# Optimization experiments

Measured on AMD Instinct MI355X. Metric: run time of the kernel, lower is better.

The kernel has to match this reference:

```python
import jax, jax.numpy as jnp
import numpy as np
from jax import lax

B, T, H, E, V, ENC = 2048, 48, 512, 256, 128, 1024


def setup_inputs() -> dict:
    key = jax.random.key(0)
    ks = jax.random.split(key, 13)
    s = 0.05  # weight scale to keep activations sane
    return {
        "tgt_ids": jax.random.randint(ks[0], (B, T), 0, V),
        "enc_hid": jax.random.normal(ks[1], (B, ENC), jnp.float32),
        "W_init1": s * jax.random.normal(ks[2], (ENC, H), jnp.float32),
        "W_init2": s * jax.random.normal(ks[3], (ENC, H), jnp.float32),
        "embed_table": s * jax.random.normal(ks[4], (V, E), jnp.float32),
        "k1": s * jax.random.normal(ks[5], (E, 3 * H), jnp.float32),
        "rk1": s * jax.random.normal(ks[6], (H, 3 * H), jnp.float32),
        "b1": jnp.zeros((2, 3 * H), jnp.float32),
        "k2": s * jax.random.normal(ks[7], (H, 3 * H), jnp.float32),
        "rk2": s * jax.random.normal(ks[8], (H, 3 * H), jnp.float32),
        "b2": jnp.zeros((2, 3 * H), jnp.float32),
        "Wv": s * jax.random.normal(ks[9], (H, V), jnp.float32),
        "bv": jnp.zeros((V,), jnp.float32),
    }


def gru_masked(x_proj, mask, h0, rk, rb):
    """Keras GRU (reset_after=True, gate order z,r,h) with mask carry-through.
    x_proj: [B,T,3H] precomputed x@kernel + input_bias. mask: [B,T] bool.
    Masked steps keep previous state AND previous output (Keras masking semantics;
    GRU output == state)."""
    def step(h, inp):
        xg, m = inp  # xg: [B,3H], m: [B]
        inner = h @ rk + rb  # [B,3H]
        xz, xr, xh = jnp.split(xg, 3, axis=-1)
        rz, rr, rh = jnp.split(inner, 3, axis=-1)
        z = jax.nn.sigmoid(xz + rz)
        r = jax.nn.sigmoid(xr + rr)
        hh = jnp.tanh(xh + r * rh)
        h_new = z * h + (1.0 - z) * hh
        h = jnp.where(m[:, None], h_new, h)
        return h, h

    _, seq = lax.scan(step, h0, (x_proj.transpose(1, 0, 2), mask.T))
    return seq.transpose(1, 0, 2)  # [B,T,H]


def reference(tgt_ids, enc_hid, W_init1, W_init2, embed_table,
              k1, rk1, b1, k2, rk2, b2, Wv, bv):
    mask = tgt_ids != 0  # mask_zero=True
    emb = embed_table[tgt_ids]  # [B,T,E]
    h01 = enc_hid @ W_init1  # Dense no-bias init of layer-1 state
    h02 = enc_hid @ W_init2
    x1 = emb @ k1 + b1[0]  # [B,T,3H]
    seq1 = gru_masked(x1, mask, h01, rk1, b1[1])
    x2 = seq1 @ k2 + b2[0]
    seq2 = gru_masked(x2, mask, h02, rk2, b2[1])
    probs = jax.nn.softmax(seq2 @ Wv + bv, axis=-1)  # [B,T,V]
    return probs
```

## Files before the change

kernel.cpp:

```cpp
#include <hip/hip_runtime.h>
#include <hip/hip_bf16.h>
#include <math.h>

#define B_   2048
#define T_   48
#define H_   512
#define E_   256
#define V_   128
#define ENC_ 1024
#define H3_  1536
#define BH_  (B_ * H_)

typedef __attribute__((ext_vector_type(8))) short bf16x8;
typedef __attribute__((ext_vector_type(4))) float f32x4;
typedef unsigned short ushort_t;

#if defined(__has_builtin)
#if __has_builtin(__builtin_amdgcn_global_load_lds)
#define HAVE_ASYNC 1
#endif
#endif
#ifndef HAVE_ASYNC
#define HAVE_ASYNC 0
#endif

__device__ __forceinline__ void stage16(const ushort_t* g, ushort_t* l, int lane)
{
#if HAVE_ASYNC
    __builtin_amdgcn_global_load_lds(
        (const __attribute__((address_space(1))) unsigned int*)g,
        (__attribute__((address_space(3))) unsigned int*)l, 16, 0, 0);
#else
    *(bf16x8*)(l + lane * 8) = *(const bf16x8*)g;
#endif
}

__device__ __forceinline__ float sigmoidf_(float x) { return 1.0f / (1.0f + expf(-x)); }

constexpr int BM = 64, BN = 64, BK = 16;

__device__ __forceinline__ void gemm_f32_body(
    const float* __restrict__ A, const float* __restrict__ Bm,
    const float* __restrict__ bias, float* __restrict__ C,
    int M, int N, int K)
{
    __shared__ float As[BK][BM + 4];
    __shared__ float Bs[BK][BN + 4];

    const int tid = threadIdx.x;
    const int bm = blockIdx.y * BM;
    const int bn = blockIdx.x * BN;
    const int tm = (tid >> 4) * 4;
    const int tn = (tid & 15) * 4;
    const int lmA = tid >> 2;
    const int lkA = (tid & 3) * 4;
    const int lkB = tid >> 4;
    const int lnB = (tid & 15) * 4;

    float acc[4][4] = {};

    for (int k0 = 0; k0 < K; k0 += BK) {
        float4 av  = *(const float4*)(A  + (size_t)(bm + lmA) * K + (k0 + lkA));
        float4 bv4 = *(const float4*)(Bm + (size_t)(k0 + lkB) * N + (bn + lnB));
        As[lkA + 0][lmA] = av.x;
        As[lkA + 1][lmA] = av.y;
        As[lkA + 2][lmA] = av.z;
        As[lkA + 3][lmA] = av.w;
        *(float4*)&Bs[lkB][lnB] = bv4;
        __syncthreads();

        #pragma unroll
        for (int k = 0; k < BK; ++k) {
            float4 a = *(const float4*)&As[k][tm];
            float4 b = *(const float4*)&Bs[k][tn];
            acc[0][0] += a.x * b.x; acc[0][1] += a.x * b.y; acc[0][2] += a.x * b.z; acc[0][3] += a.x * b.w;
            acc[1][0] += a.y * b.x; acc[1][1] += a.y * b.y; acc[1][2] += a.y * b.z; acc[1][3] += a.y * b.w;
            acc[2][0] += a.z * b.x; acc[2][1] += a.z * b.y; acc[2][2] += a.z * b.z; acc[2][3] += a.z * b.w;
            acc[3][0] += a.w * b.x; acc[3][1] += a.w * b.y; acc[3][2] += a.w * b.z; acc[3][3] += a.w * b.w;
        }
        __syncthreads();
    }

    #pragma unroll
    for (int r = 0; r < 4; ++r)
        #pragma unroll
        for (int c = 0; c < 4; ++c) {
            float v = acc[r][c];
            if (bias) v += bias[bn + tn + c];
            C[(size_t)(bm + tm + r) * N + (bn + tn + c)] = v;
        }
}

__global__ __launch_bounds__(256) void gemm_f32(
    const float* __restrict__ A, const float* __restrict__ Bm,
    const float* __restrict__ bias, float* __restrict__ C,
    int M, int N, int K)
{
    gemm_f32_body(A, Bm, bias, C, M, N, K);
}

__global__ __launch_bounds__(256) void gemm_init2(
    const float* __restrict__ A, const float* __restrict__ B0,
    const float* __restrict__ B1, float* __restrict__ C0, float* __restrict__ C1,
    int M, int N, int K)
{
    const float* Bm = blockIdx.z ? B1 : B0;
    float*       C  = blockIdx.z ? C1 : C0;
    gemm_f32_body(A, Bm, nullptr, C, M, N, K);
}

__global__ __launch_bounds__(256) void transpose_to_bf16(
    const float* __restrict__ W, __hip_bfloat16* __restrict__ Wt, int K, int N)
{
    __shared__ float tile[32][33];
    const int bk = blockIdx.y * 32, bn = blockIdx.x * 32;
    const int tx = threadIdx.x & 31, ty = threadIdx.x >> 5;
    #pragma unroll
    for (int i = ty; i < 32; i += 8)
        tile[i][tx] = W[(size_t)(bk + i) * N + (bn + tx)];
    __syncthreads();
    #pragma unroll
    for (int i = ty; i < 32; i += 8)
        Wt[(size_t)(bn + i) * K + (bk + tx)] = __float2bfloat16(tile[tx][i]);
}

__global__ __launch_bounds__(256) void f32_to_bf16_k(
    const float* __restrict__ a, __hip_bfloat16* __restrict__ o, int n)
{
    int idx = blockIdx.x * 256 + threadIdx.x;
    if (idx < n) o[idx] = __float2bfloat16(a[idx]);
}

__global__ __launch_bounds__(256, 2) void l1_fused(
    const int* __restrict__ tgt, int t,
    const float* __restrict__ xe1,
    const ushort_t* __restrict__ rkt,
    const float* __restrict__ rb,
    const float* __restrict__ hf_cur, const ushort_t* __restrict__ hb_cur,
    float* __restrict__ hf_nxt, __hip_bfloat16* __restrict__ hb_nxt)
{
    __shared__ __attribute__((aligned(16))) ushort_t Al[2][4096];
    __shared__ __attribute__((aligned(16))) ushort_t Bl[2][6144];

    const int tid  = threadIdx.x;
    const int lane = tid & 63;
    const int w    = tid >> 6;
    const int ln   = lane & 15;
    const int kg   = lane >> 4;
    const int wr   = w >> 1, wc = w & 1;

    const int lin = blockIdx.y * 16 + blockIdx.x;
    const int swz = (lin & 7) * 64 + (lin >> 3);
    const int m0  = (swz >> 4) * 64;
    const int i0  = (swz & 15) * 32;

    const int crow = lane >> 3;
    const int ckof = ((lane & 7) ^ crow) * 8;
    const int i    = i0 + wc * 16 + ln;

    const float rbz = rb[i], rbr = rb[H_ + i], rbh = rb[2 * H_ + i];
    int   ids[2][4];
    float hvs[2][4];
    #pragma unroll
    for (int fm = 0; fm < 2; ++fm)
        #pragma unroll
        for (int r = 0; r < 4; ++r) {
            const int b = m0 + wr * 32 + fm * 16 + kg * 4 + r;
            ids[fm][r] = tgt[(size_t)b * T_ + t];
            hvs[fm][r] = hf_cur[(size_t)b * H_ + i];
        }
    float xgz[2][4], xgr[2][4], xgh[2][4];
    #pragma unroll
    for (int fm = 0; fm < 2; ++fm)
        #pragma unroll
        for (int r = 0; r < 4; ++r) {
            const float* xg = xe1 + (size_t)ids[fm][r] * H3_;
            xgz[fm][r] = xg[i]; xgr[fm][r] = xg[H_ + i]; xgh[fm][r] = xg[2 * H_ + i];
        }

    const int ko0 = (kg * 8) ^ ((ln & 7) * 8);
    const int ko1 = (32 + kg * 8) ^ ((ln & 7) * 8);

    f32x4 acc[2][3] = {};

    auto STAGE = [&](int pb, int k0) {
        #pragma unroll
        for (int c = w; c < 20; c += 4) {
            const ushort_t* g; ushort_t* l;
            if (c < 8) {
                g = hb_cur + (size_t)(m0 + c * 8 + crow) * H_ + k0 + ckof;
                l = &Al[pb][c * 512];
            } else {
                const int idx = c - 8;
                g = rkt + (size_t)((idx >> 2) * H_ + i0 + (idx & 3) * 8 + crow) * H_ + k0 + ckof;
                l = &Bl[pb][idx * 512];
            }
            stage16(g, l, lane);
        }
    };

    STAGE(0, 0);
    __syncthreads();
    int buf = 0;
    for (int k0 = 0; k0 < H_; k0 += 64) {
        if (k0 + 64 < H_) STAGE(buf ^ 1, k0 + 64);
        #pragma unroll
        for (int kk = 0; kk < 2; ++kk) {
            const int ko = kk ? ko1 : ko0;
            bf16x8 af[2], bf[3];
            #pragma unroll
            for (int fm = 0; fm < 2; ++fm)
                af[fm] = *(const bf16x8*)(&Al[buf][(wr * 32 + fm * 16 + ln) * 64 + ko]);
            #pragma unroll
            for (int g = 0; g < 3; ++g)
                bf[g] = *(const bf16x8*)(&Bl[buf][g * 2048 + (wc * 16 + ln) * 64 + ko]);
            #pragma unroll
            for (int fm = 0; fm < 2; ++fm)
                #pragma unroll
                for (int g = 0; g < 3; ++g)
                    acc[fm][g] = __builtin_amdgcn_mfma_f32_16x16x32_bf16(
                        af[fm], bf[g], acc[fm][g], 0, 0, 0);
        }
        __syncthreads();
        buf ^= 1;
    }

    #pragma unroll
    for (int fm = 0; fm < 2; ++fm)
        #pragma unroll
        for (int r = 0; r < 4; ++r) {
            const int b = m0 + wr * 32 + fm * 16 + kg * 4 + r;
            const float hv = hvs[fm][r];
            float z  = sigmoidf_(xgz[fm][r] + acc[fm][0][r] + rbz);
            float rr = sigmoidf_(xgr[fm][r] + acc[fm][1][r] + rbr);
            float hh = tanhf(xgh[fm][r] + rr * (acc[fm][2][r] + rbh));
            float hn = (ids[fm][r] != 0) ? (z * hv + (1.0f - z) * hh) : hv;
            hf_nxt[(size_t)b * H_ + i] = hn;
            hb_nxt[(size_t)b * H_ + i] = __float2bfloat16(hn);
        }
}

__global__ __launch_bounds__(256, 2) void l2_fused(
    const int* __restrict__ tgt, int t,
    const ushort_t* __restrict__ k2t,
    const ushort_t* __restrict__ rk2t,
    const float* __restrict__ bx,
    const float* __restrict__ br,
    const ushort_t* __restrict__ s1b,
    const float* __restrict__ hf_cur,
    const ushort_t* __restrict__ hb_cur, size_t hbs,
    float* __restrict__ hf_nxt,
    __hip_bfloat16* __restrict__ hbo, size_t hos)
{
    __shared__ __attribute__((aligned(16))) ushort_t A0l[2][4096];
    __shared__ __attribute__((aligned(16))) ushort_t A1l[2][4096];
    __shared__ __attribute__((aligned(16))) ushort_t B0l[6144];
    __shared__ __attribute__((aligned(16))) ushort_t B1l[6144];

    const int tid  = threadIdx.x;
    const int lane = tid & 63;
    const int w    = tid >> 6;
    const int ln   = lane & 15;
    const int kg   = lane >> 4;
    const int wr   = w >> 1, wc = w & 1;

    const int lin = blockIdx.y * 16 + blockIdx.x;
    const int swz = (lin & 7) * 64 + (lin >> 3);
    const int m0  = (swz >> 4) * 64;
    const int i0  = (swz & 15) * 32;

    const int crow = lane >> 3;
    const int ckof = ((lane & 7) ^ crow) * 8;
    const int i    = i0 + wc * 16 + ln;

    const float bxz = bx[i], bxr = bx[H_ + i], bxh = bx[2 * H_ + i];
    const float brz = br[i], brr = br[H_ + i], brh = br[2 * H_ + i];
    int   ids[2][4];
    float hvs[2][4];
    #pragma unroll
    for (int fm = 0; fm < 2; ++fm)
        #pragma unroll
        for (int r = 0; r < 4; ++r) {
            const int b = m0 + wr * 32 + fm * 16 + kg * 4 + r;
            ids[fm][r] = tgt[(size_t)b * T_ + t];
            hvs[fm][r] = hf_cur[(size_t)b * H_ + i];
        }

    const int ko0 = (kg * 8) ^ ((ln & 7) * 8);
    const int ko1 = (32 + kg * 8) ^ ((ln & 7) * 8);

    auto STAGE_A = [&](int pb, int k0) {
        #pragma unroll
        for (int c = w; c < 16; c += 4) {
            const ushort_t* g; ushort_t* l;
            if (c < 8) {
                g = s1b + (size_t)(m0 + c * 8 + crow) * H_ + k0 + ckof;
                l = &A0l[pb][c * 512];
            } else {
                const int cc = c - 8;
                g = hb_cur + (size_t)(m0 + cc * 8 + crow) * hbs + k0 + ckof;
                l = &A1l[pb][cc * 512];
            }
            stage16(g, l, lane);
        }
    };
    auto STAGE_B = [&](int k0) {
        #pragma unroll
        for (int c = w; c < 24; c += 4) {
            const ushort_t* g; ushort_t* l;
            if (c < 12) {
                g = k2t + (size_t)((c >> 2) * H_ + i0 + (c & 3) * 8 + crow) * H_ + k0 + ckof;
                l = &B0l[c * 512];
            } else {
                const int idx = c - 12;
                g = rk2t + (size_t)((idx >> 2) * H_ + i0 + (idx & 3) * 8 + crow) * H_ + k0 + ckof;
                l = &B1l[idx * 512];
            }
            stage16(g, l, lane);
        }
    };

    f32x4 acc0[2][3] = {};
    f32x4 acc1[2][3] = {};

    STAGE_A(0, 0);
    STAGE_B(0);
    __syncthreads();
    int buf = 0;
    for (int k0 = 0; k0 < H_; k0 += 64) {
        const bool more = (k0 + 64 < H_);
        if (more) STAGE_A(buf ^ 1, k0 + 64);

        bf16x8 a0f[2][2], a1f[2][2], b0f[2][3], b1f[2][3];
        #pragma unroll
        for (int kk = 0; kk < 2; ++kk) {
            const int ko = kk ? ko1 : ko0;
            #pragma unroll
            for (int fm = 0; fm < 2; ++fm) {
                a0f[kk][fm] = *(const bf16x8*)(&A0l[buf][(wr * 32 + fm * 16 + ln) * 64 + ko]);
                a1f[kk][fm] = *(const bf16x8*)(&A1l[buf][(wr * 32 + fm * 16 + ln) * 64 + ko]);
            }
            #pragma unroll
            for (int g = 0; g < 3; ++g) {
                b0f[kk][g] = *(const bf16x8*)(&B0l[g * 2048 + (wc * 16 + ln) * 64 + ko]);
                b1f[kk][g] = *(const bf16x8*)(&B1l[g * 2048 + (wc * 16 + ln) * 64 + ko]);
            }
        }
        __builtin_amdgcn_sched_barrier(0);
        asm volatile("s_waitcnt lgkmcnt(0)" ::: "memory");
        __builtin_amdgcn_sched_barrier(0);
        __builtin_amdgcn_s_barrier();
        if (more) STAGE_B(k0 + 64);

        #pragma unroll
        for (int kk = 0; kk < 2; ++kk)
            #pragma unroll
            for (int fm = 0; fm < 2; ++fm)
                #pragma unroll
                for (int g = 0; g < 3; ++g) {
                    acc0[fm][g] = __builtin_amdgcn_mfma_f32_16x16x32_bf16(
                        a0f[kk][fm], b0f[kk][g], acc0[fm][g], 0, 0, 0);
                    acc1[fm][g] = __builtin_amdgcn_mfma_f32_16x16x32_bf16(
                        a1f[kk][fm], b1f[kk][g], acc1[fm][g], 0, 0, 0);
                }
        __syncthreads();
        buf ^= 1;
    }

    #pragma unroll
    for (int fm = 0; fm < 2; ++fm)
        #pragma unroll
        for (int r = 0; r < 4; ++r) {
            const int b = m0 + wr * 32 + fm * 16 + kg * 4 + r;
            const float hv = hvs[fm][r];
            float z  = sigmoidf_((acc0[fm][0][r] + bxz) + (acc1[fm][0][r] + brz));
            float rr = sigmoidf_((acc0[fm][1][r] + bxr) + (acc1[fm][1][r] + brr));
            float hh = tanhf((acc0[fm][2][r] + bxh) + rr * (acc1[fm][2][r] + brh));
            float hn = (ids[fm][r] != 0) ? (z * hv + (1.0f - z) * hh) : hv;
            hf_nxt[(size_t)b * H_ + i] = hn;
            hbo[(size_t)b * hos + i] = __float2bfloat16(hn);
        }
}

__device__ __forceinline__ void softmax_write4(
    float ax, float ay, float az, float aw, float* __restrict__ outp, int cg)
{
    float m = fmaxf(fmaxf(ax, ay), fmaxf(az, aw));
    #pragma unroll
    for (int d = 16; d >= 1; d >>= 1) m = fmaxf(m, __shfl_xor(m, d));
    float ex = __expf(ax - m), ey = __expf(ay - m),
          ez = __expf(az - m), ew = __expf(aw - m);
    float s = ex + ey + ez + ew;
    #pragma unroll
    for (int d = 16; d >= 1; d >>= 1) s += __shfl_xor(s, d);
    float inv = 1.0f / s;
    float4 o; o.x = ex * inv; o.y = ey * inv; o.z = ez * inv; o.w = ew * inv;
    *(float4*)(outp + cg * 4) = o;
}

__global__ __launch_bounds__(256) void out_softmax(
    const float* __restrict__ h2, const float* __restrict__ Wv,
    const float* __restrict__ bv, float* __restrict__ out, int t)
{
    const int tid = threadIdx.x;
    const int cg = tid & 31;
    const int rg = tid >> 5;
    const int row0 = blockIdx.x * 16;

    __shared__ float hs[16][512];
    for (int idx = tid; idx < 16 * 512; idx += 256)
        hs[idx >> 9][idx & 511] = h2[(size_t)(row0 + (idx >> 9)) * 512 + (idx & 511)];
    __syncthreads();

    const int r0 = rg * 2;
    const float4 bvv = *(const float4*)(bv + cg * 4);
    float a0x = bvv.x, a0y = bvv.y, a0z = bvv.z, a0w = bvv.w;
    float a1x = bvv.x, a1y = bvv.y, a1z = bvv.z, a1w = bvv.w;

    #pragma unroll 4
    for (int k = 0; k < 512; ++k) {
        float4 wv = *(const float4*)(Wv + (size_t)k * V_ + cg * 4);
        float h0 = hs[r0][k], h1 = hs[r0 + 1][k];
        a0x += h0 * wv.x; a0y += h0 * wv.y; a0z += h0 * wv.z; a0w += h0 * wv.w;
        a1x += h1 * wv.x; a1y += h1 * wv.y; a1z += h1 * wv.z; a1w += h1 * wv.w;
    }

    softmax_write4(a0x, a0y, a0z, a0w, out + ((size_t)(row0 + r0) * T_ + t) * V_, cg);
    softmax_write4(a1x, a1y, a1z, a1w, out + ((size_t)(row0 + r0 + 1) * T_ + t) * V_, cg);
}

__global__ __launch_bounds__(256) void proj_mfma(
    const ushort_t* __restrict__ s2, const ushort_t* __restrict__ wvt,
    const float* __restrict__ bv, float* __restrict__ out)
{
    const int lane = threadIdx.x & 63;
    const int w    = threadIdx.x >> 6;
    const int ln   = lane & 15;
    const int kg   = lane >> 4;
    const size_t row0 = (size_t)blockIdx.x * 128 + (size_t)w * 32;

    float bvl[8];
    #pragma unroll
    for (int nf = 0; nf < 8; ++nf) bvl[nf] = bv[nf * 16 + ln];

    f32x4 acc[2][8] = {};
    #pragma unroll 2
    for (int k0 = 0; k0 < H_; k0 += 32) {
        bf16x8 af[2], bf[8];
        #pragma unroll
        for (int mf = 0; mf < 2; ++mf)
            af[mf] = *(const bf16x8*)(s2 + (row0 + mf * 16 + ln) * H_ + k0 + kg * 8);
        #pragma unroll
        for (int nf = 0; nf < 8; ++nf)
            bf[nf] = *(const bf16x8*)(wvt + (size_t)(nf * 16 + ln) * H_ + k0 + kg * 8);
        #pragma unroll
        for (int mf = 0; mf < 2; ++mf)
            #pragma unroll
            for (int nf = 0; nf < 8; ++nf)
                acc[mf][nf] = __builtin_amdgcn_mfma_f32_16x16x32_bf16(
                    af[mf], bf[nf], acc[mf][nf], 0, 0, 0);
    }

    #pragma unroll
    for (int mf = 0; mf < 2; ++mf)
        #pragma unroll
        for (int q = 0; q < 4; ++q) {
            float v[8];
            float m = -1e30f;
            #pragma unroll
            for (int nf = 0; nf < 8; ++nf) { v[nf] = acc[mf][nf][q] + bvl[nf]; m = fmaxf(m, v[nf]); }
            #pragma unroll
            for (int d = 1; d <= 8; d <<= 1) m = fmaxf(m, __shfl_xor(m, d));
            float s = 0.f;
            #pragma unroll
            for (int nf = 0; nf < 8; ++nf) { v[nf] = __expf(v[nf] - m); s += v[nf]; }
            #pragma unroll
            for (int d = 1; d <= 8; d <<= 1) s += __shfl_xor(s, d);
            const float inv = 1.0f / s;
            float* op = out + (row0 + mf * 16 + kg * 4 + q) * V_;
            #pragma unroll
            for (int nf = 0; nf < 8; ++nf) op[nf * 16 + ln] = v[nf] * inv;
        }
}

extern "C" void kernel_launch(void* const* d_in, const int* in_sizes, int n_in,
                              void* d_out, int out_size, void* d_ws, size_t ws_size,
                              hipStream_t stream)
{
    const int*   tgt  = (const int*)  d_in[0];
    const float* enc  = (const float*)d_in[1];
    const float* Wi1  = (const float*)d_in[2];
    const float* Wi2  = (const float*)d_in[3];
    const float* emb  = (const float*)d_in[4];
    const float* k1   = (const float*)d_in[5];
    const float* rk1  = (const float*)d_in[6];
    const float* b1   = (const float*)d_in[7];
    const float* k2   = (const float*)d_in[8];
    const float* rk2  = (const float*)d_in[9];
    const float* b2   = (const float*)d_in[10];
    const float* Wv   = (const float*)d_in[11];
    const float* bv   = (const float*)d_in[12];
    float* out = (float*)d_out;

    float* ws  = (float*)d_ws;
    float* xe1 = ws;
    float* h1f = xe1 + (size_t)V_ * H3_;
    float* h2f = h1f + (size_t)2 * BH_;
    __hip_bfloat16* h1b = (__hip_bfloat16*)(h2f + (size_t)2 * BH_);
    __hip_bfloat16* h2b = h1b + (size_t)2 * BH_;
    __hip_bfloat16* rk1t = h2b + (size_t)2 * BH_;
    __hip_bfloat16* k2t  = rk1t + (size_t)H3_ * H_;
    __hip_bfloat16* rk2t = k2t  + (size_t)H3_ * H_;
    __hip_bfloat16* wvt  = rk2t + (size_t)H3_ * H_;
    __hip_bfloat16* seq2b = wvt + (size_t)V_ * H_;

    const size_t need = (size_t)((char*)(seq2b + (size_t)B_ * T_ * H_) - (char*)d_ws);
    const bool batched = ws_size >= need;

    dim3 blk(256);

    transpose_to_bf16<<<dim3(H3_ / 32, H_ / 32), blk, 0, stream>>>(rk1, rk1t, H_, H3_);
    transpose_to_bf16<<<dim3(H3_ / 32, H_ / 32), blk, 0, stream>>>(k2,  k2t,  H_, H3_);
    transpose_to_bf16<<<dim3(H3_ / 32, H_ / 32), blk, 0, stream>>>(rk2, rk2t, H_, H3_);
    if (batched)
        transpose_to_bf16<<<dim3(V_ / 32, H_ / 32), blk, 0, stream>>>(Wv, wvt, H_, V_);

    gemm_f32<<<dim3(H3_ / BN, V_ / BM), blk, 0, stream>>>(emb, k1, b1, xe1, V_, H3_, E_);
    gemm_init2<<<dim3(H_ / BN, B_ / BM, 2), blk, 0, stream>>>(enc, Wi1, Wi2, h1f, h2f, B_, H_, ENC_);
    f32_to_bf16_k<<<BH_ / 256, blk, 0, stream>>>(h1f, h1b, BH_);
    f32_to_bf16_k<<<BH_ / 256, blk, 0, stream>>>(h2f, h2b, BH_);

    const dim3 fgrid(H_ / 32, B_ / 64);

    for (int t = 0; t < T_; ++t) {
        const int cur = t & 1, nxt = cur ^ 1;
        float* h1f_c = h1f + (size_t)cur * BH_;
        float* h1f_n = h1f + (size_t)nxt * BH_;
        float* h2f_c = h2f + (size_t)cur * BH_;
        float* h2f_n = h2f + (size_t)nxt * BH_;
        __hip_bfloat16* h1b_c = h1b + (size_t)cur * BH_;
        __hip_bfloat16* h1b_n = h1b + (size_t)nxt * BH_;

        l1_fused<<<fgrid, blk, 0, stream>>>(
            tgt, t, xe1, (const ushort_t*)rk1t, b1 + H3_,
            h1f_c, (const ushort_t*)h1b_c, h1f_n, h1b_n);

        const ushort_t* hb_c; size_t hbs;
        __hip_bfloat16* hbo; size_t hos;
        if (batched) {
            hb_c = (t == 0) ? (const ushort_t*)h2b
                            : (const ushort_t*)(seq2b + (size_t)(t - 1) * H_);
            hbs  = (t == 0) ? (size_t)H_ : (size_t)T_ * H_;
            hbo  = seq2b + (size_t)t * H_;
            hos  = (size_t)T_ * H_;
        } else {
            hb_c = (const ushort_t*)(h2b + (size_t)cur * BH_); hbs = H_;
            hbo  = h2b + (size_t)nxt * BH_;                    hos = H_;
        }

        l2_fused<<<fgrid, blk, 0, stream>>>(
            tgt, t, (const ushort_t*)k2t, (const ushort_t*)rk2t, b2, b2 + H3_,
            (const ushort_t*)h1b_n, h2f_c, hb_c, hbs, h2f_n, hbo, hos);

        if (!batched)
            out_softmax<<<dim3(B_ / 16), blk, 0, stream>>>(h2f_n, Wv, bv, out, t);
    }

    if (batched)
        proj_mfma<<<dim3((B_ * T_) / 128), blk, 0, stream>>>(
            (const ushort_t*)seq2b, (const ushort_t*)wvt, bv, out);
}
```

Baseline: 1.540 ms.

## Fuse GRU time loop into persistent kernel with grid barriers; MFMA init GEMM

Replaces the 96 per-timestep kernel launches (l1_fused/l2_fused per step) with a single persistent kernel of 512 blocks that loops over timesteps and synchronises with an atomic-based grid barrier between layer phases. It also replaces the fp32 SIMT init-state GEMM plus separate bf16 casts with a split-bf16 (hi/lo, three MFMAs) MFMA GEMM that writes both fp32 and bf16 states directly. The aim is to remove launch overhead and the slow fp32 init GEMM. The persistent path relies on all 512 blocks being co-resident, which is checked once via an occupancy query, and adds grid-barrier spin costs.

```diff
diff --git a/kernel.cpp b/kernel.cpp
--- a/kernel.cpp
+++ b/kernel.cpp
@@ -10,6 +10,7 @@
 #define ENC_ 1024
 #define H3_  1536
 #define BH_  (B_ * H_)
+#define NBLK_ 512
 
 typedef __attribute__((ext_vector_type(8))) short bf16x8;
 typedef __attribute__((ext_vector_type(4))) float f32x4;
@@ -39,7 +40,7 @@
 
 constexpr int BM = 64, BN = 64, BK = 16;
 
-__device__ __forceinline__ void gemm_f32_body(
+__global__ __launch_bounds__(256) void gemm_f32(
     const float* __restrict__ A, const float* __restrict__ Bm,
     const float* __restrict__ bias, float* __restrict__ C,
     int M, int N, int K)
@@ -91,24 +92,6 @@
         }
 }
 
-__global__ __launch_bounds__(256) void gemm_f32(
-    const float* __restrict__ A, const float* __restrict__ Bm,
-    const float* __restrict__ bias, float* __restrict__ C,
-    int M, int N, int K)
-{
-    gemm_f32_body(A, Bm, bias, C, M, N, K);
-}
-
-__global__ __launch_bounds__(256) void gemm_init2(
-    const float* __restrict__ A, const float* __restrict__ B0,
-    const float* __restrict__ B1, float* __restrict__ C0, float* __restrict__ C1,
-    int M, int N, int K)
-{
-    const float* Bm = blockIdx.z ? B1 : B0;
-    float*       C  = blockIdx.z ? C1 : C0;
-    gemm_f32_body(A, Bm, nullptr, C, M, N, K);
-}
-
 __global__ __launch_bounds__(256) void transpose_to_bf16(
     const float* __restrict__ W, __hip_bfloat16* __restrict__ Wt, int K, int N)
 {
@@ -124,23 +107,58 @@
         Wt[(size_t)(bn + i) * K + (bk + tx)] = __float2bfloat16(tile[tx][i]);
 }
 
-__global__ __launch_bounds__(256) void f32_to_bf16_k(
-    const float* __restrict__ a, __hip_bfloat16* __restrict__ o, int n)
-{
-    int idx = blockIdx.x * 256 + threadIdx.x;
-    if (idx < n) o[idx] = __float2bfloat16(a[idx]);
-}
-
-__global__ __launch_bounds__(256, 2) void l1_fused(
-    const int* __restrict__ tgt, int t,
-    const float* __restrict__ xe1,
-    const ushort_t* __restrict__ rkt,
-    const float* __restrict__ rb,
-    const float* __restrict__ hf_cur, const ushort_t* __restrict__ hb_cur,
-    float* __restrict__ hf_nxt, __hip_bfloat16* __restrict__ hb_nxt)
-{
-    __shared__ __attribute__((aligned(16))) ushort_t Al[2][4096];
-    __shared__ __attribute__((aligned(16))) ushort_t Bl[2][6144];
+__global__ __launch_bounds__(256) void transpose_split(
+    const float* __restrict__ W, __hip_bfloat16* __restrict__ Whi,
+    __hip_bfloat16* __restrict__ Wlo, int K, int N)
+{
+    __shared__ float tile[32][33];
+    const int bk = blockIdx.y * 32, bn = blockIdx.x * 32;
+    const int tx = threadIdx.x & 31, ty = threadIdx.x >> 5;
+    #pragma unroll
+    for (int i = ty; i < 32; i += 8)
+        tile[i][tx] = W[(size_t)(bk + i) * N + (bn + tx)];
+    __syncthreads();
+    #pragma unroll
+    for (int i = ty; i < 32; i += 8) {
+        const float v = tile[tx][i];
+        const __hip_bfloat16 h = __float2bfloat16(v);
+        Whi[(size_t)(bn + i) * K + (bk + tx)] = h;
+        Wlo[(size_t)(bn + i) * K + (bk + tx)] = __float2bfloat16(v - __bfloat162float(h));
+    }
+}
+
+__global__ __launch_bounds__(256) void split_cast(
+    const float* __restrict__ x, __hip_bfloat16* __restrict__ hi,
+    __hip_bfloat16* __restrict__ lo, int n)
+{
+    const int i0 = (blockIdx.x * 256 + threadIdx.x) * 4;
+    if (i0 >= n) return;
+    const float4 v = *(const float4*)(x + i0);
+    const float vv[4] = { v.x, v.y, v.z, v.w };
+    #pragma unroll
+    for (int j = 0; j < 4; ++j) {
+        const __hip_bfloat16 h = __float2bfloat16(vv[j]);
+        hi[i0 + j] = h;
+        lo[i0 + j] = __float2bfloat16(vv[j] - __bfloat162float(h));
+    }
+}
+
+__global__ __launch_bounds__(256, 2) void init_mfma(
+    const ushort_t* __restrict__ ehi, const ushort_t* __restrict__ elo,
+    const ushort_t* __restrict__ w1hi, const ushort_t* __restrict__ w1lo,
+    const ushort_t* __restrict__ w2hi, const ushort_t* __restrict__ w2lo,
+    float* __restrict__ h1f, __hip_bfloat16* __restrict__ h1b,
+    float* __restrict__ h2f, __hip_bfloat16* __restrict__ h2b)
+{
+    const ushort_t* whi = blockIdx.z ? w2hi : w1hi;
+    const ushort_t* wlo = blockIdx.z ? w2lo : w1lo;
+    float* hf = blockIdx.z ? h2f : h1f;
+    __hip_bfloat16* hb = blockIdx.z ? h2b : h1b;
+
+    __shared__ __attribute__((aligned(16))) ushort_t Ahi[2][4096];
+    __shared__ __attribute__((aligned(16))) ushort_t Alo[2][4096];
+    __shared__ __attribute__((aligned(16))) ushort_t Bhi[2][2048];
+    __shared__ __attribute__((aligned(16))) ushort_t Blo[2][2048];
 
     const int tid  = threadIdx.x;
     const int lane = tid & 63;
@@ -148,8 +166,93 @@
     const int ln   = lane & 15;
     const int kg   = lane >> 4;
     const int wr   = w >> 1, wc = w & 1;
-
-    const int lin = blockIdx.y * 16 + blockIdx.x;
+    const int m0   = blockIdx.y * 64;
+    const int i0   = blockIdx.x * 32;
+
+    const int crow = lane >> 3;
+    const int ckof = ((lane & 7) ^ crow) * 8;
+    const int ko0 = (kg * 8) ^ ((ln & 7) * 8);
+    const int ko1 = (32 + kg * 8) ^ ((ln & 7) * 8);
+
+    auto STG = [&](int pb, int k0) {
+        #pragma unroll
+        for (int c = w; c < 24; c += 4) {
+            const ushort_t* g; ushort_t* l;
+            if (c < 8) {
+                g = ehi + (size_t)(m0 + c * 8 + crow) * ENC_ + k0 + ckof;
+                l = &Ahi[pb][c * 512];
+            } else if (c < 16) {
+                const int cc = c - 8;
+                g = elo + (size_t)(m0 + cc * 8 + crow) * ENC_ + k0 + ckof;
+                l = &Alo[pb][cc * 512];
+            } else if (c < 20) {
+                const int cc = c - 16;
+                g = whi + (size_t)(i0 + cc * 8 + crow) * ENC_ + k0 + ckof;
+                l = &Bhi[pb][cc * 512];
+            } else {
+                const int cc = c - 20;
+                g = wlo + (size_t)(i0 + cc * 8 + crow) * ENC_ + k0 + ckof;
+                l = &Blo[pb][cc * 512];
+            }
+            stage16(g, l, lane);
+        }
+    };
+
+    f32x4 acc[2] = {};
+    STG(0, 0);
+    __syncthreads();
+    int buf = 0;
+    for (int k0 = 0; k0 < ENC_; k0 += 64) {
+        if (k0 + 64 < ENC_) STG(buf ^ 1, k0 + 64);
+        #pragma unroll
+        for (int kk = 0; kk < 2; ++kk) {
+            const int ko = kk ? ko1 : ko0;
+            bf16x8 ah[2], al[2], bh, bl;
+            #pragma unroll
+            for (int fm = 0; fm < 2; ++fm) {
+                ah[fm] = *(const bf16x8*)(&Ahi[buf][(wr * 32 + fm * 16 + ln) * 64 + ko]);
+                al[fm] = *(const bf16x8*)(&Alo[buf][(wr * 32 + fm * 16 + ln) * 64 + ko]);
+            }
+            bh = *(const bf16x8*)(&Bhi[buf][(wc * 16 + ln) * 64 + ko]);
+            bl = *(const bf16x8*)(&Blo[buf][(wc * 16 + ln) * 64 + ko]);
+            #pragma unroll
+            for (int fm = 0; fm < 2; ++fm) {
+                acc[fm] = __builtin_amdgcn_mfma_f32_16x16x32_bf16(ah[fm], bh, acc[fm], 0, 0, 0);
+                acc[fm] = __builtin_amdgcn_mfma_f32_16x16x32_bf16(al[fm], bh, acc[fm], 0, 0, 0);
+                acc[fm] = __builtin_amdgcn_mfma_f32_16x16x32_bf16(ah[fm], bl, acc[fm], 0, 0, 0);
+            }
+        }
+        __syncthreads();
+        buf ^= 1;
+    }
+
+    const int i = i0 + wc * 16 + ln;
+    #pragma unroll
+    for (int fm = 0; fm < 2; ++fm)
+        #pragma unroll
+        for (int r = 0; r < 4; ++r) {
+            const int b = m0 + wr * 32 + fm * 16 + kg * 4 + r;
+            const float v = acc[fm][r];
+            hf[(size_t)b * H_ + i] = v;
+            hb[(size_t)b * H_ + i] = __float2bfloat16(v);
+        }
+}
+
+__device__ __forceinline__ void l1_phase(
+    ushort_t* Al0, ushort_t* Bl0,
+    int lin, int t,
+    const int* __restrict__ tgt, const float* __restrict__ xe1,
+    const ushort_t* __restrict__ rkt, const float* __restrict__ rb,
+    const float* __restrict__ hf_cur, const ushort_t* __restrict__ hb_cur,
+    float* __restrict__ hf_nxt, __hip_bfloat16* __restrict__ hb_nxt)
+{
+    const int tid  = threadIdx.x;
+    const int lane = tid & 63;
+    const int w    = tid >> 6;
+    const int ln   = lane & 15;
+    const int kg   = lane >> 4;
+    const int wr   = w >> 1, wc = w & 1;
+
     const int swz = (lin & 7) * 64 + (lin >> 3);
     const int m0  = (swz >> 4) * 64;
     const int i0  = (swz & 15) * 32;
@@ -189,11 +292,11 @@
             const ushort_t* g; ushort_t* l;
             if (c < 8) {
                 g = hb_cur + (size_t)(m0 + c * 8 + crow) * H_ + k0 + ckof;
-                l = &Al[pb][c * 512];
+                l = Al0 + pb * 4096 + c * 512;
             } else {
                 const int idx = c - 8;
                 g = rkt + (size_t)((idx >> 2) * H_ + i0 + (idx & 3) * 8 + crow) * H_ + k0 + ckof;
-                l = &Bl[pb][idx * 512];
+                l = Bl0 + pb * 6144 + idx * 512;
             }
             stage16(g, l, lane);
         }
@@ -210,10 +313,10 @@
             bf16x8 af[2], bf[3];
             #pragma unroll
             for (int fm = 0; fm < 2; ++fm)
-                af[fm] = *(const bf16x8*)(&Al[buf][(wr * 32 + fm * 16 + ln) * 64 + ko]);
+                af[fm] = *(const bf16x8*)(Al0 + buf * 4096 + (wr * 32 + fm * 16 + ln) * 64 + ko);
             #pragma unroll
             for (int g = 0; g < 3; ++g)
-                bf[g] = *(const bf16x8*)(&Bl[buf][g * 2048 + (wc * 16 + ln) * 64 + ko]);
+                bf[g] = *(const bf16x8*)(Bl0 + buf * 6144 + g * 2048 + (wc * 16 + ln) * 64 + ko);
             #pragma unroll
             for (int fm = 0; fm < 2; ++fm)
                 #pragma unroll
@@ -240,22 +343,21 @@
         }
 }
 
-__global__ __launch_bounds__(256, 2) void l2_fused(
-    const int* __restrict__ tgt, int t,
-    const ushort_t* __restrict__ k2t,
-    const ushort_t* __restrict__ rk2t,
-    const float* __restrict__ bx,
-    const float* __restrict__ br,
+__device__ __forceinline__ void l2_phase(
+    ushort_t* lds, int lin, int t,
+    const int* __restrict__ tgt,
+    const ushort_t* __restrict__ k2t, const ushort_t* __restrict__ rk2t,
+    const float* __restrict__ bx, const float* __restrict__ br,
     const ushort_t* __restrict__ s1b,
     const float* __restrict__ hf_cur,
     const ushort_t* __restrict__ hb_cur, size_t hbs,
     float* __restrict__ hf_nxt,
     __hip_bfloat16* __restrict__ hbo, size_t hos)
 {
-    __shared__ __attribute__((aligned(16))) ushort_t A0l[2][4096];
-    __shared__ __attribute__((aligned(16))) ushort_t A1l[2][4096];
-    __shared__ __attribute__((aligned(16))) ushort_t B0l[6144];
-    __shared__ __attribute__((aligned(16))) ushort_t B1l[6144];
+    ushort_t* A0l = lds;
+    ushort_t* A1l = lds + 8192;
+    ushort_t* B0l = lds + 16384;
+    ushort_t* B1l = lds + 22528;
 
     const int tid  = threadIdx.x;
     const int lane = tid & 63;
@@ -264,7 +366,6 @@
     const int kg   = lane >> 4;
     const int wr   = w >> 1, wc = w & 1;
 
-    const int lin = blockIdx.y * 16 + blockIdx.x;
     const int swz = (lin & 7) * 64 + (lin >> 3);
     const int m0  = (swz >> 4) * 64;
     const int i0  = (swz & 15) * 32;
@@ -295,11 +396,11 @@
             const ushort_t* g; ushort_t* l;
             if (c < 8) {
                 g = s1b + (size_t)(m0 + c * 8 + crow) * H_ + k0 + ckof;
-                l = &A0l[pb][c * 512];
+                l = A0l + pb * 4096 + c * 512;
             } else {
                 const int cc = c - 8;
                 g = hb_cur + (size_t)(m0 + cc * 8 + crow) * hbs + k0 + ckof;
-                l = &A1l[pb][cc * 512];
+                l = A1l + pb * 4096 + cc * 512;
             }
             stage16(g, l, lane);
         }
@@ -310,11 +411,11 @@
             const ushort_t* g; ushort_t* l;
             if (c < 12) {
                 g = k2t + (size_t)((c >> 2) * H_ + i0 + (c & 3) * 8 + crow) * H_ + k0 + ckof;
-                l = &B0l[c * 512];
+                l = B0l + c * 512;
             } else {
                 const int idx = c - 12;
                 g = rk2t + (size_t)((idx >> 2) * H_ + i0 + (idx & 3) * 8 + crow) * H_ + k0 + ckof;
-                l = &B1l[idx * 512];
+                l = B1l + idx * 512;
             }
             stage16(g, l, lane);
         }
@@ -337,13 +438,13 @@
             const int ko = kk ? ko1 : ko0;
             #pragma unroll
             for (int fm = 0; fm < 2; ++fm) {
-                a0f[kk][fm] = *(const bf16x8*)(&A0l[buf][(wr * 32 + fm * 16 + ln) * 64 + ko]);
-                a1f[kk][fm] = *(const bf16x8*)(&A1l[buf][(wr * 32 + fm * 16 + ln) * 64 + ko]);
+                a0f[kk][fm] = *(const bf16x8*)(A0l + buf * 4096 + (wr * 32 + fm * 16 + ln) * 64 + ko);
+                a1f[kk][fm] = *(const bf16x8*)(A1l + buf * 4096 + (wr * 32 + fm * 16 + ln) * 64 + ko);
             }
             #pragma unroll
             for (int g = 0; g < 3; ++g) {
-                b0f[kk][g] = *(const bf16x8*)(&B0l[g * 2048 + (wc * 16 + ln) * 64 + ko]);
-                b1f[kk][g] = *(const bf16x8*)(&B1l[g * 2048 + (wc * 16 + ln) * 64 + ko]);
+                b0f[kk][g] = *(const bf16x8*)(B0l + g * 2048 + (wc * 16 + ln) * 64 + ko);
+                b1f[kk][g] = *(const bf16x8*)(B1l + g * 2048 + (wc * 16 + ln) * 64 + ko);
             }
         }
         __builtin_amdgcn_sched_barrier(0);
@@ -380,6 +481,90 @@
             hf_nxt[(size_t)b * H_ + i] = hn;
             hbo[(size_t)b * hos + i] = __float2bfloat16(hn);
         }
+}
+
+__global__ __launch_bounds__(256, 2) void l1_fused(
+    const int* __restrict__ tgt, int t,
+    const float* __restrict__ xe1, const ushort_t* __restrict__ rkt,
+    const float* __restrict__ rb,
+    const float* __restrict__ hf_cur, const ushort_t* __restrict__ hb_cur,
+    float* __restrict__ hf_nxt, __hip_bfloat16* __restrict__ hb_nxt)
+{
+    __shared__ __attribute__((aligned(16))) ushort_t lds[20480];
+    l1_phase(lds, lds + 8192, blockIdx.x, t, tgt, xe1, rkt, rb,
+             hf_cur, hb_cur, hf_nxt, hb_nxt);
+}
+
+__global__ __launch_bounds__(256, 2) void l2_fused(
+    const int* __restrict__ tgt, int t,
+    const ushort_t* __restrict__ k2t, const ushort_t* __restrict__ rk2t,
+    const float* __restrict__ bx, const float* __restrict__ br,
+    const ushort_t* __restrict__ s1b,
+    const float* __restrict__ hf_cur,
+    const ushort_t* __restrict__ hb_cur, size_t hbs,
+    float* __restrict__ hf_nxt,
+    __hip_bfloat16* __restrict__ hbo, size_t hos)
+{
+    __shared__ __attribute__((aligned(16))) ushort_t lds[28672];
+    l2_phase(lds, blockIdx.x, t, tgt, k2t, rk2t, bx, br, s1b,
+             hf_cur, hb_cur, hbs, hf_nxt, hbo, hos);
+}
+
+__device__ __forceinline__ void grid_barrier(unsigned* bar)
+{
+    __syncthreads();
+    if (threadIdx.x == 0) {
+        __threadfence();
+        const unsigned g = __hip_atomic_load(&bar[1], __ATOMIC_RELAXED, __HIP_MEMORY_SCOPE_AGENT);
+        const unsigned arrived =
+            __hip_atomic_fetch_add(&bar[0], 1u, __ATOMIC_ACQ_REL, __HIP_MEMORY_SCOPE_AGENT) + 1u;
+        if (arrived == (unsigned)NBLK_) {
+            __hip_atomic_store(&bar[0], 0u, __ATOMIC_RELAXED, __HIP_MEMORY_SCOPE_AGENT);
+            __hip_atomic_store(&bar[1], g + 1u, __ATOMIC_RELEASE, __HIP_MEMORY_SCOPE_AGENT);
+        } else {
+            while (__hip_atomic_load(&bar[1], __ATOMIC_ACQUIRE, __HIP_MEMORY_SCOPE_AGENT) == g)
+                __builtin_amdgcn_s_sleep(2);
+        }
+        __threadfence();
+    }
+    __syncthreads();
+}
+
+__global__ __launch_bounds__(256, 2) void recurrence_all(
+    const int* __restrict__ tgt, const float* __restrict__ xe1,
+    const ushort_t* __restrict__ rk1t, const float* __restrict__ rb1,
+    const ushort_t* __restrict__ k2t, const ushort_t* __restrict__ rk2t,
+    const float* __restrict__ bx, const float* __restrict__ br,
+    float* __restrict__ h1f, __hip_bfloat16* __restrict__ h1b,
+    float* __restrict__ h2f, __hip_bfloat16* __restrict__ h2b,
+    __hip_bfloat16* __restrict__ seq2b, unsigned* __restrict__ bar)
+{
+    __shared__ __attribute__((aligned(16))) ushort_t lds[28672];
+    const int lin = blockIdx.x;
+
+    #pragma unroll 1
+    for (int t = 0; t < T_; ++t) {
+        const int cur = t & 1, nxt = cur ^ 1;
+
+        l1_phase(lds, lds + 8192, lin, t, tgt, xe1, rk1t, rb1,
+                 h1f + (size_t)cur * BH_,
+                 (const ushort_t*)(h1b + (size_t)cur * BH_),
+                 h1f + (size_t)nxt * BH_,
+                 h1b + (size_t)nxt * BH_);
+        grid_barrier(bar);
+
+        const ushort_t* hb_c = (t == 0)
+            ? (const ushort_t*)h2b
+            : (const ushort_t*)(seq2b + (size_t)(t - 1) * H_);
+        const size_t hbs = (t == 0) ? (size_t)H_ : (size_t)T_ * H_;
+
+        l2_phase(lds, lin, t, tgt, k2t, rk2t, bx, br,
+                 (const ushort_t*)(h1b + (size_t)nxt * BH_),
+                 h2f + (size_t)cur * BH_, hb_c, hbs,
+                 h2f + (size_t)nxt * BH_,
+                 seq2b + (size_t)t * H_, (size_t)T_ * H_);
+        grid_barrier(bar);
+    }
 }
 
 __device__ __forceinline__ void softmax_write4(
@@ -512,10 +697,28 @@
     __hip_bfloat16* k2t  = rk1t + (size_t)H3_ * H_;
     __hip_bfloat16* rk2t = k2t  + (size_t)H3_ * H_;
     __hip_bfloat16* wvt  = rk2t + (size_t)H3_ * H_;
-    __hip_bfloat16* seq2b = wvt + (size_t)V_ * H_;
-
-    const size_t need = (size_t)((char*)(seq2b + (size_t)B_ * T_ * H_) - (char*)d_ws);
+    __hip_bfloat16* ehi  = wvt + (size_t)V_ * H_;
+    __hip_bfloat16* elo  = ehi + (size_t)B_ * ENC_;
+    __hip_bfloat16* w1hi = elo + (size_t)B_ * ENC_;
+    __hip_bfloat16* w1lo = w1hi + (size_t)H_ * ENC_;
+    __hip_bfloat16* w2hi = w1lo + (size_t)H_ * ENC_;
+    __hip_bfloat16* w2lo = w2hi + (size_t)H_ * ENC_;
+    __hip_bfloat16* seq2b = w2lo + (size_t)H_ * ENC_;
+    unsigned* bar = (unsigned*)(seq2b + (size_t)B_ * T_ * H_);
+
+    const size_t need = (size_t)((char*)bar + 64 - (char*)d_ws);
     const bool batched = ws_size >= need;
+
+    static int persist_state = -1;
+    if (persist_state < 0) {
+        int nb = 0;
+        hipError_t e1 = hipOccupancyMaxActiveBlocksPerMultiprocessor(&nb, recurrence_all, 256, 0);
+        hipDeviceProp_t prop;
+        hipError_t e2 = hipGetDeviceProperties(&prop, 0);
+        persist_state = (e1 == hipSuccess && e2 == hipSuccess &&
+                         (long)nb * prop.multiProcessorCount >= NBLK_) ? 1 : 0;
+    }
+    const bool persist = batched && persist_state == 1;
 
     dim3 blk(256);
 
@@ -525,13 +728,30 @@
     if (batched)
         transpose_to_bf16<<<dim3(V_ / 32, H_ / 32), blk, 0, stream>>>(Wv, wvt, H_, V_);
 
+    split_cast<<<dim3((B_ * ENC_) / 1024), blk, 0, stream>>>(enc, ehi, elo, B_ * ENC_);
+    transpose_split<<<dim3(H_ / 32, ENC_ / 32), blk, 0, stream>>>(Wi1, w1hi, w1lo, ENC_, H_);
+    transpose_split<<<dim3(H_ / 32, ENC_ / 32), blk, 0, stream>>>(Wi2, w2hi, w2lo, ENC_, H_);
+
     gemm_f32<<<dim3(H3_ / BN, V_ / BM), blk, 0, stream>>>(emb, k1, b1, xe1, V_, H3_, E_);
-    gemm_init2<<<dim3(H_ / BN, B_ / BM, 2), blk, 0, stream>>>(enc, Wi1, Wi2, h1f, h2f, B_, H_, ENC_);
-    f32_to_bf16_k<<<BH_ / 256, blk, 0, stream>>>(h1f, h1b, BH_);
-    f32_to_bf16_k<<<BH_ / 256, blk, 0, stream>>>(h2f, h2b, BH_);
-
-    const dim3 fgrid(H_ / 32, B_ / 64);
-
+
+    init_mfma<<<dim3(H_ / 32, B_ / 64, 2), blk, 0, stream>>>(
+        (const ushort_t*)ehi, (const ushort_t*)elo,
+        (const ushort_t*)w1hi, (const ushort_t*)w1lo,
+        (const ushort_t*)w2hi, (const ushort_t*)w2lo,
+        h1f, h1b, h2f, h2b);
+
+    if (persist) {
+        hipMemsetAsync(bar, 0, 64, stream);
+        recurrence_all<<<dim3(NBLK_), blk, 0, stream>>>(
+            tgt, xe1, (const ushort_t*)rk1t, b1 + H3_,
+            (const ushort_t*)k2t, (const ushort_t*)rk2t, b2, b2 + H3_,
+            h1f, h1b, h2f, h2b, seq2b, bar);
+        proj_mfma<<<dim3((B_ * T_) / 128), blk, 0, stream>>>(
+            (const ushort_t*)seq2b, (const ushort_t*)wvt, bv, out);
+        return;
+    }
+
+    const dim3 fgrid(NBLK_);
     for (int t = 0; t < T_; ++t) {
         const int cur = t & 1, nxt = cur ^ 1;
         float* h1f_c = h1f + (size_t)cur * BH_;
```

New measurement: 1.475 ms. 1.04x faster.
